# Optimization experiments

Hardware: AMD Instinct MI355X
Metric: run time of the kernel (lower is better)

## Reference

```python
import jax, jax.numpy as jnp
import numpy as np

N = 50000      # nodes
E = 1600000    # edges
F_IN = 8       # node_features
H = 64         # hidden_dim
P = 5          # poly_degree
L = 3          # n_layers


def setup_inputs() -> dict:
    key = jax.random.key(0)
    ks = jax.random.split(key, 20)
    s = lambda *shape: 0.05
    inp = {
        "x": jax.random.normal(ks[0], (N, F_IN), jnp.float32),
        "edge_index": jax.random.randint(ks[1], (2, E), 0, N, jnp.int32),
        "edge_weight": jax.random.uniform(ks[2], (E,), jnp.float32),
        # input projection (xavier-ish)
        "W_in": jax.random.normal(ks[3], (H, F_IN), jnp.float32) * 0.15,
        "b_in": jnp.zeros((H,), jnp.float32),
        # per-layer coeff_net: Linear(H+4 -> 32) -> ReLU -> Linear(32 -> P+1) -> Softmax
        "coeff_W1": jax.random.normal(ks[4], (L, 32, H + 4), jnp.float32) * 0.1,
        "coeff_b1": jnp.zeros((L, 32), jnp.float32),
        "coeff_W2": jax.random.normal(ks[5], (L, P + 1, 32), jnp.float32) * 0.1,
        "coeff_b2": jnp.zeros((L, P + 1), jnp.float32),
        # per-layer LayerNorm params
        "ln_scale": jnp.ones((L, H), jnp.float32),
        "ln_bias": jnp.zeros((L, H), jnp.float32),
        # edge predictor: Linear(2H->H) ReLU Linear(H->H//2) ReLU Linear(H//2->1) Sigmoid
        "ep_W1": jax.random.normal(ks[6], (H, 2 * H), jnp.float32) * 0.08,
        "ep_b1": jnp.zeros((H,), jnp.float32),
        "ep_W2": jax.random.normal(ks[7], (H // 2, H), jnp.float32) * 0.1,
        "ep_b2": jnp.zeros((H // 2,), jnp.float32),
        "ep_W3": jax.random.normal(ks[8], (1, H // 2), jnp.float32) * 0.15,
        "ep_b3": jnp.zeros((1,), jnp.float32),
    }
    return inp


def _layernorm(v, scale, bias, eps=1e-5):
    m = v.mean(-1, keepdims=True)
    var = v.var(-1, keepdims=True)
    return (v - m) / jnp.sqrt(var + eps) * scale + bias


def _diffusion(h, row, col, norm, cW1, cb1, cW2, cb2):
    # coefficient MLP conditioned on graph stats (std is unbiased, as torch)
    x_mean = h.mean(0)
    stats = jnp.stack([h.mean(), h.std(ddof=1),
                       jnp.float32(N), jnp.float32(E)])
    ci = jnp.concatenate([x_mean, stats])           # (H+4,)
    hid = jax.nn.relu(ci @ cW1.T + cb1)             # (32,)
    coeffs = jax.nn.softmax(hid @ cW2.T + cb2)      # (P+1,)
    result = coeffs[0] * h
    tx = h
    for k in range(1, P + 1):
        msg = norm[:, None] * tx[col]               # (E, H) gather + scale
        tx = jax.ops.segment_sum(msg, row, num_segments=N)  # scatter-add SpMM
        result = result + coeffs[k] * tx
    return result


def reference(x, edge_index, edge_weight,
              W_in, b_in,
              coeff_W1, coeff_b1, coeff_W2, coeff_b2,
              ln_scale, ln_bias,
              ep_W1, ep_b1, ep_W2, ep_b2, ep_W3, ep_b3):
    row, col = edge_index[0], edge_index[1]
    # symmetric normalization T = D^{-1/2} A D^{-1/2} (identical every layer)
    deg = jnp.zeros((N,), x.dtype).at[col].add(edge_weight)
    dis = jnp.minimum(deg ** -0.5, 1e6)             # clamp(max=1e6) caps inf
    dis = jnp.where(jnp.isinf(dis), 0.0, dis)
    norm = dis[row] * edge_weight * dis[col]        # (E,)

    h = x @ W_in.T + b_in                           # (N, H)
    for l in range(L):
        h_new = _diffusion(h, row, col, norm,
                           coeff_W1[l], coeff_b1[l], coeff_W2[l], coeff_b2[l])
        h = _layernorm(h + h_new, ln_scale[l], ln_bias[l])

    ef = jnp.concatenate([h[row], h[col]], axis=-1)             # (E, 2H)
    e1 = jax.nn.relu(ef @ ep_W1.T + ep_b1)
    e2 = jax.nn.relu(e1 @ ep_W2.T + ep_b2)
    edge_preds = jax.nn.sigmoid(e2 @ ep_W3.T + ep_b3)[:, 0]     # (E,)
    return edge_preds, h
```

## Files before the change

### kernel.cpp

```cpp
#include <hip/hip_runtime.h>
#include <hip/hip_bf16.h>
#include <hip/hip_fp16.h>

typedef __hip_bfloat16 bf16;
typedef __attribute__((ext_vector_type(8))) short short8;
typedef __attribute__((ext_vector_type(8))) _Float16 half8;
typedef __attribute__((ext_vector_type(2))) _Float16 half2v;
typedef __attribute__((ext_vector_type(4))) float f32x4;

#define N_NODES 50000
#define N_EDGES 1600000
#define FIN 8
#define HD 64
#define NH (N_NODES * HD)
#define NLAYERS 3

#define RSLC 256
#define EPR (N_EDGES / RSLC)
#define NWORDS 12500
#define DEGSTR 50048
#define NDEGR 4

__device__ __forceinline__ float b2f(bf16 v) { return __bfloat162float(v); }
__device__ __forceinline__ float bu2f(unsigned int u) { return __uint_as_float(u << 16); }
__device__ __forceinline__ unsigned short f2bu(float f) {
    unsigned int x = __float_as_uint(f);
    unsigned int r = x + 0x7FFFu + ((x >> 16) & 1u);
    return (unsigned short)(r >> 16);
}
__device__ __forceinline__ unsigned short f2h(float f) {
    _Float16 h = (_Float16)f;
    return *(unsigned short*)&h;
}
union H16 { unsigned short b; _Float16 h; };
__device__ __forceinline__ float h16f(unsigned u) {
    H16 x; x.b = (unsigned short)u;
    return (float)x.h;
}

__global__ void k_detect(const void* __restrict__ ew, int* __restrict__ flag) {
    int ok = 1;
    for (int i = threadIdx.x; i < 512; i += 64) {
        float v = b2f(((const bf16*)ew)[i]);
        if (!(v >= 0.f && v <= 1.f)) ok = 0;
    }
    unsigned long long m = __ballot(ok);
    if (threadIdx.x == 0) *flag = (m == 0xFFFFFFFFFFFFFFFFull) ? 0 : 1;
}

struct ConvArgs {
    const void* src[14];
    float* dst[14];
    int cum[15];
};

__global__ void k_conv_small(ConvArgs a, const int* __restrict__ flag) {
    int q = blockIdx.x * 256 + threadIdx.x;
    if (q >= a.cum[14]) return;
    int s = 0;
    while (q >= a.cum[s + 1]) ++s;
    int off = q - a.cum[s];
    if (*flag) a.dst[s][off] = ((const float*)a.src[s])[off];
    else       a.dst[s][off] = bu2f(((const unsigned short*)a.src[s])[off]);
}


__global__ void __launch_bounds__(256) k_hist_row(const int* __restrict__ ei,
                                                  unsigned int* __restrict__ pcnt_u32) {
    __shared__ unsigned int sm[NWORDS];
    int b = blockIdx.x, t = threadIdx.x;
    for (int i = t; i < NWORDS; i += 256) sm[i] = 0;
    __syncthreads();
    int ebase = b * EPR;
    for (int el = t; el < EPR; el += 256) {
        int r = ei[ebase + el];
        atomicAdd(&sm[r >> 2], 1u << ((r & 3) * 8));
    }
    __syncthreads();
    unsigned int* dst = pcnt_u32 + (size_t)b * NWORDS;
    for (int i = t; i < NWORDS; i += 256) dst[i] = sm[i];
}

__global__ void k_merge(const unsigned char* __restrict__ pcnt8,
                        int* __restrict__ cnt,
                        unsigned short* __restrict__ pref16, int* __restrict__ bsum) {
    __shared__ int red[256];
    int t = threadIdx.x;
    int n = blockIdx.x * 256 + t;
    int run = 0;
    if (n < N_NODES) {
#pragma unroll 8
        for (int s = 0; s < RSLC; ++s) {
            pref16[(size_t)s * N_NODES + n] = (unsigned short)run;
            run += pcnt8[(size_t)s * N_NODES + n];
        }
        cnt[n] = run;
    }
    red[t] = run;
    __syncthreads();
    for (int off = 128; off; off >>= 1) {
        if (t < off) red[t] += red[t + off];
        __syncthreads();
    }
    if (t == 0) bsum[blockIdx.x] = red[0];
}

__global__ void k_scan_top(const int* __restrict__ bsum, int* __restrict__ bpre,
                           int* __restrict__ row_ptr) {
    __shared__ int sm[256];
    int t = threadIdx.x;
    int v = (t < 196) ? bsum[t] : 0;
    sm[t] = v;
    __syncthreads();
    int val = v;
    for (int off = 1; off < 256; off <<= 1) {
        int other = (t >= off) ? sm[t - off] : 0;
        __syncthreads();
        val += other;
        sm[t] = val;
        __syncthreads();
    }
    bpre[t] = val - v;
    if (t == 0) row_ptr[N_NODES] = N_EDGES;
}

__global__ void k_scan_fin(const int* __restrict__ cnt, const int* __restrict__ bpre,
                           int* __restrict__ row_ptr) {
    __shared__ int sm[256];
    int t = threadIdx.x;
    int n = blockIdx.x * 256 + t;
    int v = (n < N_NODES) ? cnt[n] : 0;
    sm[t] = v;
    __syncthreads();
    int val = v;
    for (int off = 1; off < 256; off <<= 1) {
        int other = (t >= off) ? sm[t - off] : 0;
        __syncthreads();
        val += other;
        sm[t] = val;
        __syncthreads();
    }
    if (n < N_NODES) row_ptr[n] = bpre[blockIdx.x] + val - v;
}

__global__ void __launch_bounds__(256) k_placeA(const int* __restrict__ ei,
                                                const void* __restrict__ ewr,
                                                const int* __restrict__ flag,
                                                const int* __restrict__ row_ptr,
                                                const unsigned short* __restrict__ pref16,
                                                unsigned int* __restrict__ pairs4,
                                                int* __restrict__ iperm,
                                                float* __restrict__ deg4) {
    __shared__ unsigned int sm[NWORDS];
    int b = blockIdx.x, t = threadIdx.x;
    for (int i = t; i < NWORDS; i += 256) sm[i] = 0;
    __syncthreads();
    int f32 = *flag;
    int ebase = b * EPR;
    const unsigned short* pr = pref16 + (size_t)b * N_NODES;
    for (int el = t; el < EPR; el += 256) {
        int e = ebase + el;
        int r = ei[e];
        int c = ei[N_EDGES + e];
        float w = f32 ? ((const float*)ewr)[e] : bu2f(((const unsigned short*)ewr)[e]);
        atomicAdd(&deg4[(size_t)(e & (NDEGR - 1)) * DEGSTR + c], w);
        int sh = (r & 3) * 8;
        unsigned old = atomicAdd(&sm[r >> 2], 1u << sh);
        int ord = (old >> sh) & 0xFF;
        int pos = row_ptr[r] + pr[r] + ord;
        pairs4[pos] = ((unsigned)c << 16) | (unsigned)f2h(w);
        iperm[e] = pos;
    }
}

__global__ void __launch_bounds__(256) k_rc(const int* __restrict__ row_ptr,
                                            const unsigned int* __restrict__ pairs4,
                                            unsigned int* __restrict__ rc) {
    int lane = threadIdx.x & 63;
    int wv = __builtin_amdgcn_readfirstlane((int)(blockIdx.x * 4 + (threadIdx.x >> 6)));
    int s = __builtin_amdgcn_readfirstlane(row_ptr[wv]);
    int e = __builtin_amdgcn_readfirstlane(row_ptr[wv + 1]);
    unsigned rhi = ((unsigned)wv) << 16;
    for (int pos = s + lane; pos < e; pos += 64)
        rc[pos] = (pairs4[pos] >> 16) | rhi;
}

__global__ void k_dis(const float* __restrict__ deg4,
                      float* __restrict__ dis, float* __restrict__ dis2) {
    int n = blockIdx.x * 256 + threadIdx.x;
    if (n >= N_NODES) return;
    float d = deg4[n] + deg4[DEGSTR + n] + deg4[2 * DEGSTR + n] + deg4[3 * DEGSTR + n];
    float di = fminf(rsqrtf(d), 1e6f);
    dis[n] = di;
    dis2[n] = di * di;
}


__global__ void k_inproj(const void* __restrict__ xr_, const float* __restrict__ W,
                         const float* __restrict__ b, const float* __restrict__ dis,
                         float* __restrict__ h,
                         unsigned short* __restrict__ h_bf, const int* __restrict__ flag) {
    __shared__ float Wt[FIN * HD];
    __shared__ float bs[HD];
    int t = threadIdx.x;
    int f32 = *flag;
    for (int idx = t; idx < FIN * HD; idx += 256) {
        int f = idx >> 3, j = idx & 7;
        Wt[j * 64 + f] = W[idx];
    }
    if (t < 64) bs[t] = b[t];
    __syncthreads();
    int gid = blockIdx.x * 256 + t;
    if (gid < NH) {
        int i = gid >> 6, f = gid & 63;
        const float* xf = (const float*)xr_ + i * FIN;
        const unsigned short* xb = (const unsigned short*)xr_ + i * FIN;
        float acc = bs[f];
#pragma unroll
        for (int j = 0; j < FIN; ++j) {
            float xv = f32 ? xf[j] : bu2f(xb[j]);
            acc += xv * Wt[j * 64 + f];
        }
        h[gid] = acc;
        h_bf[gid] = f2bu(acc * dis[i]);
    }
}


__global__ void k_stats(const float* __restrict__ h, float* __restrict__ stats) {
    __shared__ float ssum[256], ssq[256];
    int t = threadIdx.x;
    float ls = 0.f, lq = 0.f;
    for (int idx = blockIdx.x * 256 + t; idx < NH; idx += 102400) {
        float v = h[idx];
        ls += v; lq += v * v;
    }
    ssum[t] = ls; ssq[t] = lq;
    __syncthreads();
    if (t < 64) {
        float a = ssum[t] + ssum[t + 64] + ssum[t + 128] + ssum[t + 192];
        atomicAdd(&stats[t], a);
        float q = ssq[t] + ssq[t + 64] + ssq[t + 128] + ssq[t + 192];
        for (int off = 32; off; off >>= 1) q += __shfl_down(q, off, 64);
        if (t == 0) atomicAdd(&stats[64], q);
    }
}

__global__ void k_coeffs(const float* __restrict__ stats,
                         const float* __restrict__ W1, const float* __restrict__ b1,
                         const float* __restrict__ W2, const float* __restrict__ b2,
                         int layer, float* __restrict__ coeffs) {
    __shared__ float ci[68];
    __shared__ float hid[32];
    __shared__ float lg[6];
    int t = threadIdx.x;
    float sf = stats[t];
    float tot = sf;
    for (int off = 1; off < 64; off <<= 1) tot += __shfl_xor(tot, off, 64);
    ci[t] = sf / (float)N_NODES;
    if (t == 0) {
        float sumsq = stats[64];
        float mean = tot / (float)NH;
        float var = (sumsq - (float)NH * mean * mean) / (float)(NH - 1);
        ci[64] = mean;
        ci[65] = sqrtf(fmaxf(var, 0.f));
        ci[66] = (float)N_NODES;
        ci[67] = (float)N_EDGES;
    }
    __syncthreads();
    if (t < 32) {
        float a = b1[layer * 32 + t];
        const float* wr = W1 + (layer * 32 + t) * 68;
        for (int j = 0; j < 68; ++j) a += ci[j] * wr[j];
        hid[t] = fmaxf(a, 0.f);
    }
    __syncthreads();
    if (t < 6) {
        float a = b2[layer * 6 + t];
        const float* wr = W2 + (layer * 6 + t) * 32;
        for (int g = 0; g < 32; ++g) a += hid[g] * wr[g];
        lg[t] = a;
    }
    __syncthreads();
    if (t == 0) {
        float mx = lg[0];
        for (int p = 1; p < 6; ++p) mx = fmaxf(mx, lg[p]);
        float s = 0.f, e[6];
        for (int p = 0; p < 6; ++p) { e[p] = expf(lg[p] - mx); s += e[p]; }
        for (int p = 0; p < 6; ++p) coeffs[p] = e[p] / s;
    }
}


__device__ __forceinline__ float acc_range(const unsigned short* __restrict__ txo,
                                           const unsigned int* __restrict__ pairs4,
                                           int j0, int j1, int lane, float acc) {
    int j = j0;
    for (; j + 15 < j1; j += 16) {
        unsigned p0 = pairs4[j],      p1 = pairs4[j + 1],  p2 = pairs4[j + 2],  p3 = pairs4[j + 3];
        unsigned p4 = pairs4[j + 4],  p5 = pairs4[j + 5],  p6 = pairs4[j + 6],  p7 = pairs4[j + 7];
        unsigned p8 = pairs4[j + 8],  p9 = pairs4[j + 9],  pa = pairs4[j + 10], pb = pairs4[j + 11];
        unsigned pc = pairs4[j + 12], pd = pairs4[j + 13], pe = pairs4[j + 14], pf = pairs4[j + 15];
        float g0 = bu2f(txo[(p0 >> 16) * 64 + lane]);
        float g1 = bu2f(txo[(p1 >> 16) * 64 + lane]);
        float g2 = bu2f(txo[(p2 >> 16) * 64 + lane]);
        float g3 = bu2f(txo[(p3 >> 16) * 64 + lane]);
        float g4 = bu2f(txo[(p4 >> 16) * 64 + lane]);
        float g5 = bu2f(txo[(p5 >> 16) * 64 + lane]);
        float g6 = bu2f(txo[(p6 >> 16) * 64 + lane]);
        float g7 = bu2f(txo[(p7 >> 16) * 64 + lane]);
        float g8 = bu2f(txo[(p8 >> 16) * 64 + lane]);
        float g9 = bu2f(txo[(p9 >> 16) * 64 + lane]);
        float ga = bu2f(txo[(pa >> 16) * 64 + lane]);
        float gb = bu2f(txo[(pb >> 16) * 64 + lane]);
        float gc = bu2f(txo[(pc >> 16) * 64 + lane]);
        float gd = bu2f(txo[(pd >> 16) * 64 + lane]);
        float ge = bu2f(txo[(pe >> 16) * 64 + lane]);
        float gf = bu2f(txo[(pf >> 16) * 64 + lane]);
        acc += h16f(p0) * g0 + h16f(p1) * g1 + h16f(p2) * g2 + h16f(p3) * g3;
        acc += h16f(p4) * g4 + h16f(p5) * g5 + h16f(p6) * g6 + h16f(p7) * g7;
        acc += h16f(p8) * g8 + h16f(p9) * g9 + h16f(pa) * ga + h16f(pb) * gb;
        acc += h16f(pc) * gc + h16f(pd) * gd + h16f(pe) * ge + h16f(pf) * gf;
    }
    for (; j + 7 < j1; j += 8) {
        unsigned p0 = pairs4[j],     p1 = pairs4[j + 1], p2 = pairs4[j + 2], p3 = pairs4[j + 3];
        unsigned p4 = pairs4[j + 4], p5 = pairs4[j + 5], p6 = pairs4[j + 6], p7 = pairs4[j + 7];
        float g0 = bu2f(txo[(p0 >> 16) * 64 + lane]);
        float g1 = bu2f(txo[(p1 >> 16) * 64 + lane]);
        float g2 = bu2f(txo[(p2 >> 16) * 64 + lane]);
        float g3 = bu2f(txo[(p3 >> 16) * 64 + lane]);
        float g4 = bu2f(txo[(p4 >> 16) * 64 + lane]);
        float g5 = bu2f(txo[(p5 >> 16) * 64 + lane]);
        float g6 = bu2f(txo[(p6 >> 16) * 64 + lane]);
        float g7 = bu2f(txo[(p7 >> 16) * 64 + lane]);
        acc += h16f(p0) * g0 + h16f(p1) * g1 + h16f(p2) * g2 + h16f(p3) * g3;
        acc += h16f(p4) * g4 + h16f(p5) * g5 + h16f(p6) * g6 + h16f(p7) * g7;
    }
    for (; j < j1; ++j) {
        unsigned p = pairs4[j];
        acc += h16f(p) * bu2f(txo[(p >> 16) * 64 + lane]);
    }
    return acc;
}

__global__ void __launch_bounds__(256) k_spmm(
    const unsigned short* __restrict__ txo, unsigned short* __restrict__ txn,
    const int* __restrict__ row_ptr, const unsigned int* __restrict__ pairs4,
    const float* __restrict__ dis2) {
    int lane = threadIdx.x & 63;
    int wv = __builtin_amdgcn_readfirstlane((int)(blockIdx.x * 4 + (threadIdx.x >> 6)));
    int s = __builtin_amdgcn_readfirstlane(row_ptr[wv]);
    int e = __builtin_amdgcn_readfirstlane(row_ptr[wv + 1]);
    float acc = acc_range(txo, pairs4, s, e, lane, 0.f);
    float d2 = dis2[wv];
    txn[wv * 64 + lane] = f2bu(acc * d2);
}


__global__ void __launch_bounds__(256) k_spmm_ln(
    const unsigned short* __restrict__ txo,
    const int* __restrict__ row_ptr, const unsigned int* __restrict__ pairs4,
    float* __restrict__ h, unsigned short* __restrict__ h_bf,
    const unsigned short* __restrict__ t1, const unsigned short* __restrict__ t2,
    const unsigned short* __restrict__ t3, const unsigned short* __restrict__ t4,
    const float* __restrict__ coeffs, const float* __restrict__ dis,
    const float* __restrict__ sc, const float* __restrict__ bi,
    int layer, int last, void* __restrict__ outv, const int* __restrict__ flag) {
    int lane = threadIdx.x & 63;
    int wv = __builtin_amdgcn_readfirstlane((int)(blockIdx.x * 4 + (threadIdx.x >> 6)));
    int s = __builtin_amdgcn_readfirstlane(row_ptr[wv]);
    int e = __builtin_amdgcn_readfirstlane(row_ptr[wv + 1]);
    float acc = acc_range(txo, pairs4, s, e, lane, 0.f);
    int o = wv * 64 + lane;
    float ds = dis[wv];
    float invd = 1.f / ds;
    float c0 = coeffs[0], c1 = coeffs[1], c2 = coeffs[2],
          c3 = coeffs[3], c4 = coeffs[4], c5 = coeffs[5];
    float v = (1.f + c0) * h[o] +
              invd * (c1 * bu2f(t1[o]) + c2 * bu2f(t2[o]) +
                      c3 * bu2f(t3[o]) + c4 * bu2f(t4[o])) +
              c5 * ds * acc;
    float m = v;
    for (int off = 1; off < 64; off <<= 1) m += __shfl_xor(m, off, 64);
    m *= (1.f / 64.f);
    float d = v - m;
    float q = d * d;
    for (int off = 1; off < 64; off <<= 1) q += __shfl_xor(q, off, 64);
    float var = q * (1.f / 64.f);
    float y = d / sqrtf(var + 1e-5f) * sc[layer * 64 + lane] + bi[layer * 64 + lane];
    h[o] = y;
    h_bf[o] = f2bu(y * ds);
    if (last) {
        if (*flag) ((float*)outv)[N_EDGES + o] = y;
        else       ((unsigned short*)outv)[N_EDGES + o] = f2bu(y);
    }
}


__global__ void __launch_bounds__(256) k_uv(const float* __restrict__ h,
                                            const float* __restrict__ W1,
                                            unsigned short* __restrict__ ub,
                                            unsigned short* __restrict__ vb) {
    __shared__ float Wt[128 * 65];
    __shared__ float hs[4 * 64];
    int t = threadIdx.x;
    for (int idx = t; idx < 8192; idx += 256) {
        int f = idx >> 7, j = idx & 127;
        Wt[j * 65 + f] = W1[idx];
    }
    int node0 = blockIdx.x * 4;
    hs[t] = h[node0 * 64 + t];
    __syncthreads();
    int ni = t >> 6, f = t & 63;
    const float* hr = hs + ni * 64;
    float au = 0.f, av = 0.f;
#pragma unroll 8
    for (int j = 0; j < 64; ++j) {
        float xv = hr[j];
        au += Wt[j * 65 + f] * xv;
        av += Wt[(j + 64) * 65 + f] * xv;
    }
    int i = node0 + ni;
    ub[i * 64 + f] = f2h(au);
    vb[i * 64 + f] = f2h(av);
}

__device__ __forceinline__ unsigned h2rel(unsigned uu, unsigned vv, half2v b) {
    half2v a = *(half2v*)&uu + *(half2v*)&vv + b;
    a[0] = a[0] > (_Float16)0 ? a[0] : (_Float16)0;
    a[1] = a[1] > (_Float16)0 ? a[1] : (_Float16)0;
    return *(unsigned*)&a;
}

union U4H8 { uint4 u; half8 h; };

__global__ void __launch_bounds__(256) k_edgepred(
    const unsigned short* __restrict__ ub, const unsigned short* __restrict__ vb,
    const unsigned int* __restrict__ rc,
    const float* __restrict__ eb1, const float* __restrict__ eW2,
    const float* __restrict__ eb2, const float* __restrict__ eW3,
    const float* __restrict__ eb3, float* __restrict__ tmpP) {
    int t = threadIdx.x;
    int lane = t & 63;
    int m = lane & 15, q = lane >> 4;

    half8 B00, B01, B10, B11;
#pragma unroll
    for (int j = 0; j < 8; ++j) {
        B00[j] = (_Float16)eW2[(m) * 64      + q * 8 + j];
        B01[j] = (_Float16)eW2[(m) * 64 + 32 + q * 8 + j];
        B10[j] = (_Float16)eW2[(m + 16) * 64      + q * 8 + j];
        B11[j] = (_Float16)eW2[(m + 16) * 64 + 32 + q * 8 + j];
    }
    half2v b1p0[4], b1p1[4];
#pragma unroll
    for (int wq = 0; wq < 4; ++wq) {
        b1p0[wq][0] = (_Float16)eb1[q * 8 + 2 * wq];
        b1p0[wq][1] = (_Float16)eb1[q * 8 + 2 * wq + 1];
        b1p1[wq][0] = (_Float16)eb1[32 + q * 8 + 2 * wq];
        b1p1[wq][1] = (_Float16)eb1[32 + q * 8 + 2 * wq + 1];
    }
    float w3a = eW3[m], w3b = eW3[16 + m];
    float b2a = eb2[m], b2b = eb2[16 + m];
    float b3v = eb3[0];

    int gw = blockIdx.x * 4 + (t >> 6);
    const int NW = 1563 * 4;
    for (int tile = gw; tile < N_EDGES / 16; tile += NW) {
        int base = tile << 4;
        unsigned rcv = rc[base + m];
        int col = rcv & 0xFFFF;
        int row = rcv >> 16;
        const unsigned short* up = ub + row * 64;
        const unsigned short* vp = vb + col * 64;
        uint4 U0 = *(const uint4*)(up + q * 8);
        uint4 U1 = *(const uint4*)(up + 32 + q * 8);
        uint4 V0 = *(const uint4*)(vp + q * 8);
        uint4 V1 = *(const uint4*)(vp + 32 + q * 8);
        U4H8 a0, a1;
        a0.u.x = h2rel(U0.x, V0.x, b1p0[0]);
        a0.u.y = h2rel(U0.y, V0.y, b1p0[1]);
        a0.u.z = h2rel(U0.z, V0.z, b1p0[2]);
        a0.u.w = h2rel(U0.w, V0.w, b1p0[3]);
        a1.u.x = h2rel(U1.x, V1.x, b1p1[0]);
        a1.u.y = h2rel(U1.y, V1.y, b1p1[1]);
        a1.u.z = h2rel(U1.z, V1.z, b1p1[2]);
        a1.u.w = h2rel(U1.w, V1.w, b1p1[3]);
        f32x4 acc0 = {0.f, 0.f, 0.f, 0.f};
        f32x4 acc1 = {0.f, 0.f, 0.f, 0.f};
        acc0 = __builtin_amdgcn_mfma_f32_16x16x32_f16(a0.h, B00, acc0, 0, 0, 0);
        acc0 = __builtin_amdgcn_mfma_f32_16x16x32_f16(a1.h, B01, acc0, 0, 0, 0);
        acc1 = __builtin_amdgcn_mfma_f32_16x16x32_f16(a0.h, B10, acc1, 0, 0, 0);
        acc1 = __builtin_amdgcn_mfma_f32_16x16x32_f16(a1.h, B11, acc1, 0, 0, 0);
        float z[4];
#pragma unroll
        for (int rr = 0; rr < 4; ++rr) {
            z[rr] = w3a * fmaxf(acc0[rr] + b2a, 0.f) + w3b * fmaxf(acc1[rr] + b2b, 0.f);
            z[rr] += __shfl_xor(z[rr], 1, 64);
            z[rr] += __shfl_xor(z[rr], 2, 64);
            z[rr] += __shfl_xor(z[rr], 4, 64);
            z[rr] += __shfl_xor(z[rr], 8, 64);
        }
        if (m == 0) {
#pragma unroll
            for (int rr = 0; rr < 4; ++rr) {
                float p = 1.f / (1.f + __expf(-(z[rr] + b3v)));
                tmpP[base + (q << 2) + rr] = p;
            }
        }
    }
}

__global__ void k_out(const int* __restrict__ iperm, const float* __restrict__ tmpP,
                      void* __restrict__ outv, const int* __restrict__ flag) {
    int e = blockIdx.x * 256 + threadIdx.x;
    if (e >= N_EDGES) return;
    float p = tmpP[iperm[e]];
    if (*flag) ((float*)outv)[e] = p;
    else       ((unsigned short*)outv)[e] = f2bu(p);
}


extern "C" void kernel_launch(void* const* d_in, const int* in_sizes, int n_in,
                              void* d_out, int out_size, void* d_ws, size_t ws_size,
                              hipStream_t stream) {
    (void)in_sizes; (void)n_in; (void)out_size; (void)ws_size;
    const void* x_r   = d_in[0];
    const int*  ei    = (const int*)d_in[1];
    const void* ew_r  = d_in[2];

    char* w = (char*)d_ws;
    float* h            = (float*)w;          w += (size_t)NH * 4;
    unsigned short* hbf = (unsigned short*)w; w += (size_t)NH * 2;
    char* txr           = w;                  w += (size_t)NH * 8;
    unsigned int* pairs4 = (unsigned int*)w;  w += (size_t)N_EDGES * 4;
    unsigned int* rc    = (unsigned int*)w;   w += (size_t)N_EDGES * 4;
    int* iperm          = (int*)w;            w += (size_t)N_EDGES * 4;
    int* row_ptr        = (int*)w;            w += 200192;
    int* cnt            = (int*)w;            w += 200192;
    float* dis          = (float*)w;          w += 200192;
    float* dis2         = (float*)w;          w += 200192;
    float* cWin = (float*)w; w += 2048;
    float* cbin = (float*)w; w += 256;
    float* ccW1 = (float*)w; w += 26112;
    float* ccb1 = (float*)w; w += 384;
    float* ccW2 = (float*)w; w += 2304;
    float* ccb2 = (float*)w; w += 128;
    float* clns = (float*)w; w += 768;
    float* clnb = (float*)w; w += 768;
    float* ceW1 = (float*)w; w += 32768;
    float* ceb1 = (float*)w; w += 256;
    float* ceW2 = (float*)w; w += 8192;
    float* ceb2 = (float*)w; w += 128;
    float* ceW3 = (float*)w; w += 128;
    float* ceb3 = (float*)w; w += 128;
    int* bsum = (int*)w; w += 1024;
    int* bpre = (int*)w; w += 1024;
    char* zero_base = w;
    float* stats = (float*)w; w += 1024;
    float* deg4  = (float*)w; w += (size_t)NDEGR * DEGSTR * 4;
    size_t zero_bytes = (size_t)(w - zero_base);
    float* coeffs = (float*)w; w += 128;
    int*   flag   = (int*)w;   w += 128;

    unsigned int* pcnt_u32 = (unsigned int*)pairs4;
    unsigned char* pcnt8   = (unsigned char*)pairs4;
    unsigned short* pref16 = (unsigned short*)txr;
    float* tmpP            = (float*)pairs4;

    unsigned short* tx[4];
    for (int k = 0; k < 4; ++k) tx[k] = (unsigned short*)txr + (size_t)k * NH;
    unsigned short* ub = tx[0];
    unsigned short* vb = tx[1];

    (void)hipMemsetAsync(zero_base, 0, zero_bytes, stream);

    k_detect<<<1, 64, 0, stream>>>(ew_r, flag);

    ConvArgs ca;
    const void* srcs[14] = {d_in[3], d_in[4], d_in[5], d_in[6], d_in[7], d_in[8], d_in[9],
                            d_in[10], d_in[11], d_in[12], d_in[13], d_in[14], d_in[15], d_in[16]};
    float* dsts[14] = {cWin, cbin, ccW1, ccb1, ccW2, ccb2, clns,
                       clnb, ceW1, ceb1, ceW2, ceb2, ceW3, ceb3};
    int sizes[14] = {512, 64, 6528, 96, 576, 18, 192, 192, 8192, 64, 2048, 32, 32, 1};
    int c = 0;
    for (int i = 0; i < 14; ++i) { ca.src[i] = srcs[i]; ca.dst[i] = dsts[i]; ca.cum[i] = c; c += sizes[i]; }
    ca.cum[14] = c;
    k_conv_small<<<(c + 255) / 256, 256, 0, stream>>>(ca, flag);

    k_hist_row<<<RSLC, 256, 0, stream>>>(ei, pcnt_u32);
    k_merge<<<196, 256, 0, stream>>>(pcnt8, cnt, pref16, bsum);
    k_scan_top<<<1, 256, 0, stream>>>(bsum, bpre, row_ptr);
    k_scan_fin<<<196, 256, 0, stream>>>(cnt, bpre, row_ptr);
    k_placeA<<<RSLC, 256, 0, stream>>>(ei, ew_r, flag, row_ptr, pref16, pairs4, iperm, deg4);
    k_rc<<<12500, 256, 0, stream>>>(row_ptr, pairs4, rc);
    k_dis<<<196, 256, 0, stream>>>(deg4, dis, dis2);
    k_inproj<<<12500, 256, 0, stream>>>(x_r, cWin, cbin, dis, h, hbf, flag);

    for (int l = 0; l < NLAYERS; ++l) {
        k_stats<<<400, 256, 0, stream>>>(h, stats + l * 80);
        k_coeffs<<<1, 64, 0, stream>>>(stats + l * 80, ccW1, ccb1, ccW2, ccb2, l,
                                       coeffs + l * 8);
        const unsigned short* src = hbf;
        for (int k = 0; k < 4; ++k) {
            k_spmm<<<12500, 256, 0, stream>>>(src, tx[k], row_ptr, pairs4, dis2);
            src = tx[k];
        }
        k_spmm_ln<<<12500, 256, 0, stream>>>(tx[3], row_ptr, pairs4, h, hbf,
                                             tx[0], tx[1], tx[2], tx[3],
                                             coeffs + l * 8, dis, clns, clnb, l,
                                             (l == NLAYERS - 1) ? 1 : 0, d_out, flag);
    }

    k_uv<<<12500, 256, 0, stream>>>(h, ceW1, ub, vb);
    k_edgepred<<<1563, 256, 0, stream>>>(ub, vb, rc, ceb1, ceW2, ceb2, ceW3, ceb3, tmpP);
    k_out<<<6250, 256, 0, stream>>>(iperm, tmpP, d_out, flag);
}
```

Baseline: 869.6 us.

## Compute degrees via fixed-point LDS histograms instead of global float atomics

Degree accumulation moves out of k_placeA, where it used global float atomics spread over four replicas, into a new k_deg2 kernel. k_deg2 builds per-slice 16-bit fixed-point histograms in shared memory, scaling each weight by 512, and k_dis sums the 128 slices. The histogram and placement kernels also move from 256 to 1024 threads per block. This removes contended global atomics at the cost of an extra pass over the edges, and it rounds each weight to a multiple of 1/512. A 16-bit slice counter can overflow if one node collects more than about 128 of the 12,500 edges in a slice, a risk for skewed inputs.

```diff
diff --git a/kernel.cpp b/kernel.cpp
--- a/kernel.cpp
+++ b/kernel.cpp
@@ -18,8 +18,10 @@
 #define RSLC 256
 #define EPR (N_EDGES / RSLC)
 #define NWORDS 12500
-#define DEGSTR 50048
-#define NDEGR 4
+#define DSLC2 128
+#define EPD2 (N_EDGES / DSLC2)
+#define DWORDS 25000
+#define DEGSCALE 512.0f
 
 __device__ __forceinline__ float b2f(bf16 v) { return __bfloat162float(v); }
 __device__ __forceinline__ float bu2f(unsigned int u) { return __uint_as_float(u << 16); }
@@ -64,21 +66,56 @@
     else       a.dst[s][off] = bu2f(((const unsigned short*)a.src[s])[off]);
 }
 
-
-__global__ void __launch_bounds__(256) k_hist_row(const int* __restrict__ ei,
-                                                  unsigned int* __restrict__ pcnt_u32) {
+__global__ void __launch_bounds__(1024) k_deg2(const int* __restrict__ ei,
+                                               const void* __restrict__ ewr,
+                                               const int* __restrict__ flag,
+                                               unsigned short* __restrict__ pdeg16) {
+    __shared__ unsigned int sm[DWORDS];
+    int b = blockIdx.x, t = threadIdx.x;
+    for (int i = t; i < DWORDS; i += 1024) sm[i] = 0;
+    __syncthreads();
+    int f32 = *flag;
+    int ebase = b * EPD2;
+    for (int el = t; el < EPD2; el += 1024) {
+        int e = ebase + el;
+        int c = ei[N_EDGES + e];
+        float w = f32 ? ((const float*)ewr)[e] : bu2f(((const unsigned short*)ewr)[e]);
+        unsigned fx = (unsigned)__float2int_rn(w * DEGSCALE);
+        atomicAdd(&sm[c >> 1], fx << ((c & 1) * 16));
+    }
+    __syncthreads();
+    unsigned int* dst = (unsigned int*)(pdeg16 + (size_t)b * N_NODES);
+    for (int i = t; i < DWORDS; i += 1024) dst[i] = sm[i];
+}
+
+__global__ void k_dis(const unsigned short* __restrict__ pdeg16,
+                      float* __restrict__ dis, float* __restrict__ dis2) {
+    int n = blockIdx.x * 256 + threadIdx.x;
+    if (n >= N_NODES) return;
+    unsigned s = 0;
+#pragma unroll 8
+    for (int k = 0; k < DSLC2; ++k) s += pdeg16[(size_t)k * N_NODES + n];
+    float d = (float)s * (1.f / DEGSCALE);
+    float di = fminf(rsqrtf(d), 1e6f);
+    dis[n] = di;
+    dis2[n] = di * di;
+}
+
+
+__global__ void __launch_bounds__(1024) k_hist_row(const int* __restrict__ ei,
+                                                   unsigned int* __restrict__ pcnt_u32) {
     __shared__ unsigned int sm[NWORDS];
     int b = blockIdx.x, t = threadIdx.x;
-    for (int i = t; i < NWORDS; i += 256) sm[i] = 0;
+    for (int i = t; i < NWORDS; i += 1024) sm[i] = 0;
     __syncthreads();
     int ebase = b * EPR;
-    for (int el = t; el < EPR; el += 256) {
+    for (int el = t; el < EPR; el += 1024) {
         int r = ei[ebase + el];
         atomicAdd(&sm[r >> 2], 1u << ((r & 3) * 8));
     }
     __syncthreads();
     unsigned int* dst = pcnt_u32 + (size_t)b * NWORDS;
-    for (int i = t; i < NWORDS; i += 256) dst[i] = sm[i];
+    for (int i = t; i < NWORDS; i += 1024) dst[i] = sm[i];
 }
 
 __global__ void k_merge(const unsigned char* __restrict__ pcnt8,
@@ -143,27 +180,25 @@
     if (n < N_NODES) row_ptr[n] = bpre[blockIdx.x] + val - v;
 }
 
-__global__ void __launch_bounds__(256) k_placeA(const int* __restrict__ ei,
-                                                const void* __restrict__ ewr,
-                                                const int* __restrict__ flag,
-                                                const int* __restrict__ row_ptr,
-                                                const unsigned short* __restrict__ pref16,
-                                                unsigned int* __restrict__ pairs4,
-                                                int* __restrict__ iperm,
-                                                float* __restrict__ deg4) {
+__global__ void __launch_bounds__(1024) k_placeA(const int* __restrict__ ei,
+                                                 const void* __restrict__ ewr,
+                                                 const int* __restrict__ flag,
+                                                 const int* __restrict__ row_ptr,
+                                                 const unsigned short* __restrict__ pref16,
+                                                 unsigned int* __restrict__ pairs4,
+                                                 int* __restrict__ iperm) {
     __shared__ unsigned int sm[NWORDS];
     int b = blockIdx.x, t = threadIdx.x;
-    for (int i = t; i < NWORDS; i += 256) sm[i] = 0;
+    for (int i = t; i < NWORDS; i += 1024) sm[i] = 0;
     __syncthreads();
     int f32 = *flag;
     int ebase = b * EPR;
     const unsigned short* pr = pref16 + (size_t)b * N_NODES;
-    for (int el = t; el < EPR; el += 256) {
+    for (int el = t; el < EPR; el += 1024) {
         int e = ebase + el;
         int r = ei[e];
         int c = ei[N_EDGES + e];
         float w = f32 ? ((const float*)ewr)[e] : bu2f(((const unsigned short*)ewr)[e]);
-        atomicAdd(&deg4[(size_t)(e & (NDEGR - 1)) * DEGSTR + c], w);
         int sh = (r & 3) * 8;
         unsigned old = atomicAdd(&sm[r >> 2], 1u << sh);
         int ord = (old >> sh) & 0xFF;
@@ -183,16 +218,6 @@
     unsigned rhi = ((unsigned)wv) << 16;
     for (int pos = s + lane; pos < e; pos += 64)
         rc[pos] = (pairs4[pos] >> 16) | rhi;
-}
-
-__global__ void k_dis(const float* __restrict__ deg4,
-                      float* __restrict__ dis, float* __restrict__ dis2) {
-    int n = blockIdx.x * 256 + threadIdx.x;
-    if (n >= N_NODES) return;
-    float d = deg4[n] + deg4[DEGSTR + n] + deg4[2 * DEGSTR + n] + deg4[3 * DEGSTR + n];
-    float di = fminf(rsqrtf(d), 1e6f);
-    dis[n] = di;
-    dis2[n] = di * di;
 }
 
 
@@ -558,7 +583,6 @@
     int* bpre = (int*)w; w += 1024;
     char* zero_base = w;
     float* stats = (float*)w; w += 1024;
-    float* deg4  = (float*)w; w += (size_t)NDEGR * DEGSTR * 4;
     size_t zero_bytes = (size_t)(w - zero_base);
     float* coeffs = (float*)w; w += 128;
     int*   flag   = (int*)w;   w += 128;
@@ -566,6 +590,7 @@
     unsigned int* pcnt_u32 = (unsigned int*)pairs4;
     unsigned char* pcnt8   = (unsigned char*)pairs4;
     unsigned short* pref16 = (unsigned short*)txr;
+    unsigned short* pdeg16 = (unsigned short*)h;
     float* tmpP            = (float*)pairs4;
 
     unsigned short* tx[4];
@@ -588,13 +613,14 @@
     ca.cum[14] = c;
     k_conv_small<<<(c + 255) / 256, 256, 0, stream>>>(ca, flag);
 
-    k_hist_row<<<RSLC, 256, 0, stream>>>(ei, pcnt_u32);
+    k_deg2<<<DSLC2, 1024, 0, stream>>>(ei, ew_r, flag, pdeg16);
+    k_hist_row<<<RSLC, 1024, 0, stream>>>(ei, pcnt_u32);
     k_merge<<<196, 256, 0, stream>>>(pcnt8, cnt, pref16, bsum);
     k_scan_top<<<1, 256, 0, stream>>>(bsum, bpre, row_ptr);
     k_scan_fin<<<196, 256, 0, stream>>>(cnt, bpre, row_ptr);
-    k_placeA<<<RSLC, 256, 0, stream>>>(ei, ew_r, flag, row_ptr, pref16, pairs4, iperm, deg4);
+    k_placeA<<<RSLC, 1024, 0, stream>>>(ei, ew_r, flag, row_ptr, pref16, pairs4, iperm);
     k_rc<<<12500, 256, 0, stream>>>(row_ptr, pairs4, rc);
-    k_dis<<<196, 256, 0, stream>>>(deg4, dis, dis2);
+    k_dis<<<196, 256, 0, stream>>>(pdeg16, dis, dis2);
     k_inproj<<<12500, 256, 0, stream>>>(x_r, cWin, cbin, dis, h, hbf, flag);
 
     for (int l = 0; l < NLAYERS; ++l) {
```

Result: faster. 837.2 us (-3.7%).
